# Performance work log

Hardware: AMD Instinct MI355X
Metric: run time of the kernel (lower is better)

## Reference

```python
import jax, jax.numpy as jnp
import numpy as np

BATCH = 256
B_TYPES = 32   # input capsule types
C_TYPES = 10   # output capsule types
H, W = 8, 8    # input spatial extent == kernel (output is 1x1)
POSE = 16      # capsule pose length (shape (16,1))
NUM_ITER = 3
EPS = 1e-8


def setup_inputs() -> dict:
    key = jax.random.key(0)
    k1, k2, k3 = jax.random.split(key, 3)
    input_caps_poses = jax.random.normal(k1, (BATCH, B_TYPES, H, W, POSE, 1), jnp.float32)
    input_caps_activations = jax.random.uniform(k2, (BATCH, B_TYPES, H, W), jnp.float32)
    # nn.init.normal_(std=0.1) on [B, kh, kw, C, os0, is0]
    weight = 0.1 * jax.random.normal(k3, (B_TYPES, H, W, C_TYPES, POSE, POSE), jnp.float32)
    # routing_bias initialized to 0.1: [C, oh, ow, os0, os1]
    routing_bias = jnp.full((C_TYPES, 1, 1, POSE, 1), 0.1, jnp.float32)
    return {
        "input_caps_poses": input_caps_poses,
        "input_caps_activations": input_caps_activations,
        "weight": weight,
        "routing_bias": routing_bias,
    }


def _squash(s):
    # Hinton squash: ||s||^2/(1+||s||^2) * s/||s||, norm over pose dims
    n2 = jnp.sum(s * s, axis=(-2, -1), keepdims=True)
    return (n2 / (1.0 + n2)) * s * jax.lax.rsqrt(n2 + EPS)


def reference(input_caps_poses, input_caps_activations, weight, routing_bias):
    b = input_caps_poses.shape[0]
    # votes[b,c,B,h,w,o,p] = sum_i W[B,h,w,c,o,i] * pose[b,B,h,w,i,p]
    votes = jnp.einsum('Bhwcoi,bBhwip->bcBhwop', weight, input_caps_poses)
    logits = jnp.zeros((b, C_TYPES, B_TYPES, H, W), votes.dtype)
    bias = routing_bias.reshape(1, C_TYPES, POSE, 1)
    v = None
    for it in range(NUM_ITER):
        # coupling coefficients: softmax over output capsule types
        c = jax.nn.softmax(logits, axis=1)                      # [b,C,B,h,w]
        # weighted sum of votes over all input capsules (B,h,w)
        s = jnp.einsum('bcBhw,bcBhwop->bcop', c, votes) + bias  # [b,C,16,1]
        v = _squash(s)
        if it < NUM_ITER - 1:
            # agreement: dot(vote, output pose)
            logits = logits + jnp.einsum('bcBhwop,bcop->bcBhw', votes, v)
    output_caps_poses = v[:, :, None, None, :, :]               # [b,C,1,1,16,1]
    output_caps_activations = jnp.sqrt(
        jnp.sum(v * v, axis=(-2, -1)) + EPS)[:, :, None, None]  # [b,C,1,1]
    return output_caps_poses, output_caps_activations
```

## Files before the change

kernel.cpp:

```cpp
#include <hip/hip_runtime.h>
#include <hip/hip_fp16.h>
#include <math.h>


typedef _Float16 f16;
typedef _Float16 f16x2 __attribute__((ext_vector_type(2)));
typedef _Float16 f16x4 __attribute__((ext_vector_type(4)));
typedef __fp16   h16x2 __attribute__((ext_vector_type(2)));
typedef float f32x4 __attribute__((ext_vector_type(4)));

__device__ __forceinline__ f16x2 pk(float a, float b) {
    h16x2 t = __builtin_amdgcn_cvt_pkrtz(a, b);
    return __builtin_bit_cast(f16x2, t);
}

#if __has_builtin(__builtin_amdgcn_fdot2)
__device__ __forceinline__ float FDOT2(f16x2 a, f16x2 b, float c) {
    return __builtin_amdgcn_fdot2(__builtin_bit_cast(h16x2, a),
                                  __builtin_bit_cast(h16x2, b), c, false);
}
#else
__device__ __forceinline__ float FDOT2(f16x2 a, f16x2 b, float c) {
    return c + (float)a[0] * (float)b[0] + (float)a[1] * (float)b[1];
}
#endif

constexpr int WS_ROW = 28;
constexpr int XS_ROW = 76;

__device__ __forceinline__ float xorsum4(float v) {
    v += __shfl_xor(v, 16, 64);
    v += __shfl_xor(v, 32, 64);
    return v;
}

__device__ __forceinline__ f16x2 xorsum4h(f16x2 v) {
    union { f16x2 h; int i; } u;
    union { int i; f16x2 h; } w;
    u.h = v; w.i = __shfl_xor(u.i, 16, 64); v = v + w.h;
    u.h = v; w.i = __shfl_xor(u.i, 32, 64); v = v + w.h;
    return v;
}

__device__ __forceinline__ f16x4 cvt4(float4 w) {
    f16x2 a = pk(w.x, w.y);
    f16x2 b = pk(w.z, w.w);
    f16x4 r; r[0] = a[0]; r[1] = a[1]; r[2] = b[0]; r[3] = b[1];
    return r;
}

template<int PASS>
__global__ __launch_bounds__(256, 2)
void pass_k(const float* __restrict__ poses, const float* __restrict__ weight,
            const float* __restrict__ bias,
            const float* __restrict__ sp0, const float* __restrict__ sp1,
            float* __restrict__ s_dst)
{
    __shared__ f16 Ws[640 * WS_ROW];
    __shared__ f16 xs[64 * XS_ROW];

    const int tid  = threadIdx.x;
    const int blk  = blockIdx.x;
    const int ngrp = blk >> 2;
    const int b0   = (blk & 3) * 64;
    const int wave = tid >> 6;
    const int lane = tid & 63;
    const int q    = lane >> 4;
    const int lo   = lane & 15;
    const int wtb  = wave * 16;
    const int bg   = b0 + wtb;

    f16x2 vsp[10][2];
    if (PASS >= 1) {
        const int rowb = (bg + lo) * 10;
        #pragma unroll
        for (int c = 0; c < 10; ++c) {
            float4 bb = *(const float4*)(bias + c * 16 + q * 4);
            float4 sa = *(const float4*)(sp0 + (size_t)(rowb + c) * 16 + q * 4);
            float t0 = sa.x + bb.x, t1 = sa.y + bb.y, t2 = sa.z + bb.z, t3 = sa.w + bb.w;
            float n2 = xorsum4(t0*t0 + t1*t1 + t2*t2 + t3*t3);
            float sc = n2 / (1.f + n2) * rsqrtf(n2 + 1e-8f);
            float v0 = sc*t0, v1 = sc*t1, v2 = sc*t2, v3 = sc*t3;
            if (PASS == 2) {
                float4 sb = *(const float4*)(sp1 + (size_t)(rowb + c) * 16 + q * 4);
                float u0 = sb.x + bb.x, u1 = sb.y + bb.y, u2 = sb.z + bb.z, u3 = sb.w + bb.w;
                float m2 = xorsum4(u0*u0 + u1*u1 + u2*u2 + u3*u3);
                float sc2 = m2 / (1.f + m2) * rsqrtf(m2 + 1e-8f);
                v0 += sc2*u0; v1 += sc2*u1; v2 += sc2*u2; v3 += sc2*u3;
            }
            vsp[c][0] = pk(v0, v1);
            vsp[c][1] = pk(v2, v3);
        }
    }

    float4 wreg[10];
    float4 xreg[4];
    const int b_loc = tid >> 2, part = tid & 3;

    auto load_iter = [&](int l) {
        const float* wp = weight + (size_t)(ngrp * 4 + l) * 10240;
        #pragma unroll
        for (int k = 0; k < 10; ++k) wreg[k] = ((const float4*)wp)[tid + k * 256];
        const float* xp = poses + (size_t)(b0 + b_loc) * 32768
                          + (size_t)(ngrp * 16 + l * 4 + part) * 16;
        #pragma unroll
        for (int j = 0; j < 4; ++j) xreg[j] = ((const float4*)xp)[j];
    };
    auto store_iter = [&]() {
        #pragma unroll
        for (int k = 0; k < 10; ++k) {
            const int f = tid + k * 256;
            *(f16x4*)&Ws[(f >> 2) * WS_ROW + (f & 3) * 4] = cvt4(wreg[k]);
        }
        f16* lp = xs + b_loc * XS_ROW + part * 16;
        #pragma unroll
        for (int j = 0; j < 4; ++j) *(f16x4*)&lp[j * 4] = cvt4(xreg[j]);
    };

    f32x4 acc[10];
    #pragma unroll
    for (int c = 0; c < 10; ++c) acc[c] = (f32x4){0.f, 0.f, 0.f, 0.f};

    load_iter(0);

    for (int l = 0; l < 4; ++l) {
        __syncthreads();
        store_iter();
        if (l + 1 < 4) load_iter(l + 1);
        __syncthreads();

        #pragma unroll
        for (int n = 0; n < 4; ++n) {
            f16x4 bx = *(const f16x4*)&xs[(wtb + lo) * XS_ROW + n * 16 + q * 4];
            f16x2 Vh[10][2];
            #pragma unroll
            for (int c = 0; c < 10; ++c) {
                f16x4 aw = *(const f16x4*)&Ws[((n * 10 + c) * 16 + lo) * WS_ROW + q * 4];
                f32x4 V = __builtin_amdgcn_mfma_f32_16x16x16f16(
                    aw, bx, (f32x4){0.f, 0.f, 0.f, 0.f}, 0, 0, 0);
                Vh[c][0] = pk(V[0], V[1]);
                Vh[c][1] = pk(V[2], V[3]);
            }

            float cfv[10];
            if (PASS >= 1) {
                float lg[10];
                #pragma unroll
                for (int cp = 0; cp < 5; ++cp) {
                    const int c0 = cp * 2, c1 = cp * 2 + 1;
                    float p0 = FDOT2(Vh[c0][0], vsp[c0][0], 0.f);
                    p0 = FDOT2(Vh[c0][1], vsp[c0][1], p0);
                    float p1 = FDOT2(Vh[c1][0], vsp[c1][0], 0.f);
                    p1 = FDOT2(Vh[c1][1], vsp[c1][1], p1);
                    f16x2 pr = xorsum4h(pk(p0, p1));
                    lg[c0] = (float)pr[0];
                    lg[c1] = (float)pr[1];
                }
                float m = lg[0];
                #pragma unroll
                for (int c = 1; c < 10; ++c) m = fmaxf(m, lg[c]);
                float sum = 0.f;
                #pragma unroll
                for (int c = 0; c < 10; ++c) { lg[c] = __expf(lg[c] - m); sum += lg[c]; }
                const float inv = 1.f / sum;
                #pragma unroll
                for (int c = 0; c < 10; ++c) cfv[c] = lg[c] * inv;
            }

            #pragma unroll
            for (int c = 0; c < 10; ++c) {
                const float w = (PASS == 0) ? 1.f : cfv[c];
                acc[c][0] = fmaf(w, (float)Vh[c][0][0], acc[c][0]);
                acc[c][1] = fmaf(w, (float)Vh[c][0][1], acc[c][1]);
                acc[c][2] = fmaf(w, (float)Vh[c][1][0], acc[c][2]);
                acc[c][3] = fmaf(w, (float)Vh[c][1][1], acc[c][3]);
            }
        }
    }

    __syncthreads();
    float* tr = (float*)Ws + wave * 320;
    const float fs = (PASS == 0) ? 0.1f : 1.f;
    #pragma unroll
    for (int c = 0; c < 10; ++c) {
        *(float4*)&tr[lo * 20 + q * 4] = (float4){acc[c][0], acc[c][1], acc[c][2], acc[c][3]};
        float r0 = tr[(q * 4 + 0) * 20 + lo];
        float r1 = tr[(q * 4 + 1) * 20 + lo];
        float r2 = tr[(q * 4 + 2) * 20 + lo];
        float r3 = tr[(q * 4 + 3) * 20 + lo];
        float* sp = s_dst + ((size_t)(bg + q * 4) * 10 + c) * 16 + lo;
        unsafeAtomicAdd(sp + 0 * 160, fs * r0);
        unsafeAtomicAdd(sp + 1 * 160, fs * r1);
        unsafeAtomicAdd(sp + 2 * 160, fs * r2);
        unsafeAtomicAdd(sp + 3 * 160, fs * r3);
    }
}

__global__ __launch_bounds__(256)
void epi_k(const float* __restrict__ s2, const float* __restrict__ bias,
           float* __restrict__ out)
{
    const int t = blockIdx.x * 256 + threadIdx.x;
    if (t >= 2560) return;
    const int c = t % 10;
    const float* sp = s2 + (size_t)t * 16;
    const float* bp = bias + c * 16;
    float sv[16];
    float n2 = 0.f;
    #pragma unroll
    for (int o = 0; o < 16; ++o) { float v = sp[o] + bp[o]; sv[o] = v; n2 += v * v; }
    const float scale = n2 / (1.f + n2) * rsqrtf(n2 + 1e-8f);
    float a2 = 0.f;
    #pragma unroll
    for (int o = 0; o < 16; ++o) {
        float v = scale * sv[o];
        out[(size_t)t * 16 + o] = v;
        a2 += v * v;
    }
    out[40960 + t] = sqrtf(a2 + 1e-8f);
}

extern "C" void kernel_launch(void* const* d_in, const int* in_sizes, int n_in,
                              void* d_out, int out_size, void* d_ws, size_t ws_size,
                              hipStream_t stream)
{
    const float* poses  = (const float*)d_in[0];
    const float* weight = (const float*)d_in[2];
    const float* bias   = (const float*)d_in[3];
    float* out = (float*)d_out;
    float* s0 = (float*)d_ws;
    float* s1 = s0 + 40960;
    float* s2 = s1 + 40960;

    (void)hipMemsetAsync(d_ws, 0, 3 * 40960 * sizeof(float), stream);

    pass_k<0><<<512, 256, 0, stream>>>(poses, weight, bias, nullptr, nullptr, s0);
    pass_k<1><<<512, 256, 0, stream>>>(poses, weight, bias, s0, nullptr, s1);
    pass_k<2><<<512, 256, 0, stream>>>(poses, weight, bias, s0, s1, s2);
    epi_k<<<10, 256, 0, stream>>>(s2, bias, out);
}
```

Before: 203.5 us.

## Split each block's positions across two wave groups with LDS reduction

Doubles the block to 512 threads (8 waves). Two wave groups each handle half of the spatial positions per stage, so each wave does half the MFMA and softmax work, and their partial accumulators are combined through LDS before the atomic writeback. Each group owns five output types in that writeback, which halves the atomics issued per wave. The aim is more waves per CU for latency hiding and less serial work per wave, at the cost of an extra barrier, an LDS exchange and tighter register limits from launch_bounds(512,4).

After: 259.9 us. 27.7% more time.

```diff
diff --git a/kernel.cpp b/kernel.cpp
--- a/kernel.cpp
+++ b/kernel.cpp
@@ -6,6 +6,7 @@
 typedef _Float16 f16;
 typedef _Float16 f16x2 __attribute__((ext_vector_type(2)));
 typedef _Float16 f16x4 __attribute__((ext_vector_type(4)));
+typedef _Float16 f16x8 __attribute__((ext_vector_type(8)));
 typedef __fp16   h16x2 __attribute__((ext_vector_type(2)));
 typedef float f32x4 __attribute__((ext_vector_type(4)));
 
@@ -50,14 +51,17 @@
 }
 
 template<int PASS>
-__global__ __launch_bounds__(256, 2)
+__global__ __launch_bounds__(512, 4)
 void pass_k(const float* __restrict__ poses, const float* __restrict__ weight,
             const float* __restrict__ bias,
             const float* __restrict__ sp0, const float* __restrict__ sp1,
             float* __restrict__ s_dst)
 {
-    __shared__ f16 Ws[640 * WS_ROW];
-    __shared__ f16 xs[64 * XS_ROW];
+    __shared__ __align__(16) char ldsbuf[45568];
+    f16* Ws = (f16*)ldsbuf;
+    f16* xs = (f16*)(ldsbuf + 35840);
+    float* trA = (float*)ldsbuf;
+    float* trB = (float*)(ldsbuf + 20480);
 
     const int tid  = threadIdx.x;
     const int blk  = blockIdx.x;
@@ -67,7 +71,9 @@
     const int lane = tid & 63;
     const int q    = lane >> 4;
     const int lo   = lane & 15;
-    const int wtb  = wave * 16;
+    const int t    = wave & 3;
+    const int g    = wave >> 2;
+    const int wtb  = t * 16;
     const int bg   = b0 + wtb;
 
     f16x2 vsp[10][2];
@@ -93,28 +99,28 @@
         }
     }
 
-    float4 wreg[10];
-    float4 xreg[4];
-    const int b_loc = tid >> 2, part = tid & 3;
+    float4 wreg[5];
+    float4 xreg[2];
+    const int b_loc = tid >> 3, part = tid & 7;
 
     auto load_iter = [&](int l) {
         const float* wp = weight + (size_t)(ngrp * 4 + l) * 10240;
         #pragma unroll
-        for (int k = 0; k < 10; ++k) wreg[k] = ((const float4*)wp)[tid + k * 256];
+        for (int k = 0; k < 5; ++k) wreg[k] = ((const float4*)wp)[tid + k * 512];
         const float* xp = poses + (size_t)(b0 + b_loc) * 32768
-                          + (size_t)(ngrp * 16 + l * 4 + part) * 16;
-        #pragma unroll
-        for (int j = 0; j < 4; ++j) xreg[j] = ((const float4*)xp)[j];
+                          + (size_t)(ngrp * 16 + l * 4) * 16 + part * 8;
+        xreg[0] = ((const float4*)xp)[0];
+        xreg[1] = ((const float4*)xp)[1];
     };
     auto store_iter = [&]() {
         #pragma unroll
-        for (int k = 0; k < 10; ++k) {
-            const int f = tid + k * 256;
+        for (int k = 0; k < 5; ++k) {
+            const int f = tid + k * 512;
             *(f16x4*)&Ws[(f >> 2) * WS_ROW + (f & 3) * 4] = cvt4(wreg[k]);
         }
-        f16* lp = xs + b_loc * XS_ROW + part * 16;
-        #pragma unroll
-        for (int j = 0; j < 4; ++j) *(f16x4*)&lp[j * 4] = cvt4(xreg[j]);
+        f16x4 r0 = cvt4(xreg[0]), r1 = cvt4(xreg[1]);
+        f16x8 r = __builtin_shufflevector(r0, r1, 0, 1, 2, 3, 4, 5, 6, 7);
+        *(f16x8*)&xs[b_loc * XS_ROW + part * 8] = r;
     };
 
     f32x4 acc[10];
@@ -130,7 +136,8 @@
         __syncthreads();
 
         #pragma unroll
-        for (int n = 0; n < 4; ++n) {
+        for (int j = 0; j < 2; ++j) {
+            const int n = g * 2 + j;
             f16x4 bx = *(const f16x4*)&xs[(wtb + lo) * XS_ROW + n * 16 + q * 4];
             f16x2 Vh[10][2];
             #pragma unroll
@@ -179,20 +186,41 @@
     }
 
     __syncthreads();
-    float* tr = (float*)Ws + wave * 320;
-    const float fs = (PASS == 0) ? 0.1f : 1.f;
-    #pragma unroll
-    for (int c = 0; c < 10; ++c) {
-        *(float4*)&tr[lo * 20 + q * 4] = (float4){acc[c][0], acc[c][1], acc[c][2], acc[c][3]};
-        float r0 = tr[(q * 4 + 0) * 20 + lo];
-        float r1 = tr[(q * 4 + 1) * 20 + lo];
-        float r2 = tr[(q * 4 + 2) * 20 + lo];
-        float r3 = tr[(q * 4 + 3) * 20 + lo];
-        float* sp = s_dst + ((size_t)(bg + q * 4) * 10 + c) * 16 + lo;
-        unsafeAtomicAdd(sp + 0 * 160, fs * r0);
-        unsafeAtomicAdd(sp + 1 * 160, fs * r1);
-        unsafeAtomicAdd(sp + 2 * 160, fs * r2);
-        unsafeAtomicAdd(sp + 3 * 160, fs * r3);
+    {
+        float* tw = g ? trA : trB;
+        const int cgive = g ? 0 : 5;
+        #pragma unroll
+        for (int cc = 0; cc < 5; ++cc) {
+            const int idx = ((t * 5 + cc) * 16 + lo) * 4 + q;
+            *(f32x4*)&tw[idx * 4] = acc[cgive + cc];
+        }
+    }
+    __syncthreads();
+    {
+        float* td = g ? trB : trA;
+        const int ckeep = g ? 5 : 0;
+        f32x4 cmb[5];
+        #pragma unroll
+        for (int cc = 0; cc < 5; ++cc) {
+            const int idx = ((t * 5 + cc) * 16 + lo) * 4 + q;
+            f32x4 p = *(const f32x4*)&td[idx * 4];
+            cmb[cc] = acc[ckeep + cc] + p;
+        }
+        float* scr = td + t * 1280;
+        const float fs = (PASS == 0) ? 0.1f : 1.f;
+        #pragma unroll
+        for (int cc = 0; cc < 5; ++cc) {
+            *(f32x4*)&scr[lo * 20 + q * 4] = cmb[cc];
+            float r0 = scr[(q * 4 + 0) * 20 + lo];
+            float r1 = scr[(q * 4 + 1) * 20 + lo];
+            float r2 = scr[(q * 4 + 2) * 20 + lo];
+            float r3 = scr[(q * 4 + 3) * 20 + lo];
+            float* sp = s_dst + ((size_t)(bg + q * 4) * 10 + ckeep + cc) * 16 + lo;
+            unsafeAtomicAdd(sp + 0 * 160, fs * r0);
+            unsafeAtomicAdd(sp + 1 * 160, fs * r1);
+            unsafeAtomicAdd(sp + 2 * 160, fs * r2);
+            unsafeAtomicAdd(sp + 3 * 160, fs * r3);
+        }
     }
 }
 
@@ -234,8 +262,8 @@
 
     (void)hipMemsetAsync(d_ws, 0, 3 * 40960 * sizeof(float), stream);
 
-    pass_k<0><<<512, 256, 0, stream>>>(poses, weight, bias, nullptr, nullptr, s0);
-    pass_k<1><<<512, 256, 0, stream>>>(poses, weight, bias, s0, nullptr, s1);
-    pass_k<2><<<512, 256, 0, stream>>>(poses, weight, bias, s0, s1, s2);
+    pass_k<0><<<512, 512, 0, stream>>>(poses, weight, bias, nullptr, nullptr, s0);
+    pass_k<1><<<512, 512, 0, stream>>>(poses, weight, bias, s0, nullptr, s1);
+    pass_k<2><<<512, 512, 0, stream>>>(poses, weight, bias, s0, s1, s2);
     epi_k<<<10, 256, 0, stream>>>(s2, bias, out);
 }
```
